# Optimization experiments

Hardware: AMD Instinct MI355X
Metric: run time of the kernel (lower is better)

The kernel has to match this reference:

```python
import jax, jax.numpy as jnp
import numpy as np

B, L, N, D = 256, 200, 256, 16
K = 8  # fixed dopri5 substeps per output interval (replaces adaptive step control)
LN_EPS = 1e-5


def setup_inputs() -> dict:
    key = jax.random.key(0)
    ks = jax.random.split(key, 16)

    def w(k, i, o):
        return (jax.random.normal(k, (i, o), jnp.float32) / np.float32(np.sqrt(i)))

    return {
        "x_seq": jax.random.normal(ks[0], (B, L, N), jnp.float32),
        "tvec": jnp.arange(L, dtype=jnp.float32) * 0.05,
        "eps": jax.random.normal(ks[1], (B, D), jnp.float32),
        # encoder
        "enc_w1": w(ks[2], N, 512), "enc_b1": jnp.zeros((512,), jnp.float32),
        "enc_w2": w(ks[3], 512, 256), "enc_b2": jnp.zeros((256,), jnp.float32),
        "enc_w3": w(ks[4], 256, 128), "enc_b3": jnp.zeros((128,), jnp.float32),
        "mu_w": w(ks[5], 128, D), "mu_b": jnp.zeros((D,), jnp.float32),
        "lv_w": w(ks[6], 128, D), "lv_b": jnp.zeros((D,), jnp.float32),
        # latent ODE func
        "ode_w1": w(ks[7], D, 128), "ode_b1": jnp.zeros((128,), jnp.float32),
        "ode_w2": w(ks[8], 128, 128), "ode_b2": jnp.zeros((128,), jnp.float32),
        "ode_w3": w(ks[9], 128, D), "ode_b3": jnp.zeros((D,), jnp.float32),
        "ln_g": jnp.ones((D,), jnp.float32), "ln_b": jnp.zeros((D,), jnp.float32),
        # decoder
        "dec_w1": w(ks[10], D, 512), "dec_b1": jnp.zeros((512,), jnp.float32),
        "dec_w2": w(ks[11], 512, 512), "dec_b2": jnp.zeros((512,), jnp.float32),
        "dec_w3": w(ks[12], 512, N), "dec_b3": jnp.zeros((N,), jnp.float32),
    }


def _forward(x_seq, tvec, eps,
             enc_w1, enc_b1, enc_w2, enc_b2, enc_w3, enc_b3,
             mu_w, mu_b, lv_w, lv_b,
             ode_w1, ode_b1, ode_w2, ode_b2, ode_w3, ode_b3, ln_g, ln_b,
             dec_w1, dec_b1, dec_w2, dec_b2, dec_w3, dec_b3):
    # ---- encode x0 -> (mu, logvar), reparameterize ----
    x0 = x_seq[:, 0, :]                                   # [B, N]
    h = jax.nn.relu(x0 @ enc_w1 + enc_b1)
    h = jax.nn.relu(h @ enc_w2 + enc_b2)
    h = jax.nn.relu(h @ enc_w3 + enc_b3)
    mu = h @ mu_w + mu_b                                  # [B, D]
    logvar = h @ lv_w + lv_b                              # [B, D]
    z0 = mu + jnp.exp(0.5 * logvar) * eps                 # [B, D]

    # ---- latent ODE dynamics f(z) (t-independent) ----
    def f(z):
        a = jax.nn.silu(z @ ode_w1 + ode_b1)
        a = jax.nn.silu(a @ ode_w2 + ode_b2)
        dz = a @ ode_w3 + ode_b3
        m = jnp.mean(dz, axis=-1, keepdims=True)
        v = jnp.mean(jnp.square(dz - m), axis=-1, keepdims=True)
        return (dz - m) * jax.lax.rsqrt(v + LN_EPS) * ln_g + ln_b

    # ---- dopri5 (RK45) step with step size hstep ----
    def dopri_step(z, hstep):
        k1 = f(z)
        k2 = f(z + hstep * (k1 / 5.0))
        k3 = f(z + hstep * (3.0 / 40.0 * k1 + 9.0 / 40.0 * k2))
        k4 = f(z + hstep * (44.0 / 45.0 * k1 - 56.0 / 15.0 * k2 + 32.0 / 9.0 * k3))
        k5 = f(z + hstep * (19372.0 / 6561.0 * k1 - 25360.0 / 2187.0 * k2
                            + 64448.0 / 6561.0 * k3 - 212.0 / 729.0 * k4))
        k6 = f(z + hstep * (9017.0 / 3168.0 * k1 - 355.0 / 33.0 * k2
                            + 46732.0 / 5247.0 * k3 + 49.0 / 176.0 * k4
                            - 5103.0 / 18656.0 * k5))
        return z + hstep * (35.0 / 384.0 * k1 + 500.0 / 1113.0 * k3
                            + 125.0 / 192.0 * k4 - 2187.0 / 6784.0 * k5
                            + 11.0 / 84.0 * k6)

    dts = tvec[1:] - tvec[:-1]                            # [L-1]

    def interval(z, dt):
        hsub = dt / K
        def sub(zc, _):
            return dopri_step(zc, hsub), None
        z_next, _ = jax.lax.scan(sub, z, None, length=K)
        return z_next, z_next

    _, zs = jax.lax.scan(interval, z0, dts)               # [L-1, B, D]
    z_traj = jnp.concatenate([z0[None], zs], axis=0)      # [L, B, D]
    z_traj = jnp.transpose(z_traj, (1, 0, 2))             # [B, L, D]

    dt3 = dts.reshape(1, -1, 1)
    zdiff = (z_traj[:, 1:, :] - z_traj[:, :-1, :]) / dt3  # [B, L-1, D]

    # ---- decode trajectory ----
    g = jax.nn.relu(z_traj @ dec_w1 + dec_b1)
    g = jax.nn.relu(g @ dec_w2 + dec_b2)
    xhat = g @ dec_w3 + dec_b3                            # [B, L, N]
    return xhat, mu, logvar, z_traj, zdiff


def reference(x_seq, tvec, eps,
              enc_w1, enc_b1, enc_w2, enc_b2, enc_w3, enc_b3,
              mu_w, mu_b, lv_w, lv_b,
              ode_w1, ode_b1, ode_w2, ode_b2, ode_w3, ode_b3, ln_g, ln_b,
              dec_w1, dec_b1, dec_w2, dec_b2, dec_w3, dec_b3):
    return _forward(x_seq, tvec, eps,
                    enc_w1, enc_b1, enc_w2, enc_b2, enc_w3, enc_b3,
                    mu_w, mu_b, lv_w, lv_b,
                    ode_w1, ode_b1, ode_w2, ode_b2, ode_w3, ode_b3, ln_g, ln_b,
                    dec_w1, dec_b1, dec_w2, dec_b2, dec_w3, dec_b3)
```

## Files before the change

kernel.cpp:

```cpp
#include <hip/hip_runtime.h>

#define OFF_MU   13107200
#define OFF_LV   13111296
#define OFF_ZT   13115392
#define OFF_ZD   13934592

typedef float v2f __attribute__((ext_vector_type(2)));

__device__ __forceinline__ float silu_f(float x) {
    return x / (1.0f + __expf(-x));
}

__device__ __forceinline__ float readlane_f(float v, int l) {
    return __uint_as_float(__builtin_amdgcn_readlane(__float_as_uint(v), l));
}

__device__ __forceinline__ v2f fma2(v2f a, v2f b, v2f c) {
    return __builtin_elementwise_fma(a, b, c);
}

template <int CTRL>
__device__ __forceinline__ float dppadd(float x) {
    int y = __builtin_amdgcn_update_dpp(0, __float_as_int(x), CTRL, 0xF, 0xF, true);
    return x + __int_as_float(y);
}

__device__ __forceinline__ float sum16_dpp(float x) {
    x = dppadd<0xB1>(x);
    x = dppadd<0x4E>(x);
    x = dppadd<0x141>(x);
    x = dppadd<0x140>(x);
    return x;
}

__global__ __launch_bounds__(256) void enc_kernel(
    const float* __restrict__ xseq, const float* __restrict__ eps,
    const float* __restrict__ w1, const float* __restrict__ b1,
    const float* __restrict__ w2, const float* __restrict__ b2,
    const float* __restrict__ w3, const float* __restrict__ b3,
    const float* __restrict__ muw, const float* __restrict__ mub,
    const float* __restrict__ lvw, const float* __restrict__ lvb,
    float* __restrict__ out)
{
    __shared__ float xr[256];
    __shared__ float h1[512];
    __shared__ float h2[256];
    __shared__ float h3[128];

    const int t = threadIdx.x;
    const int b = blockIdx.x;

    xr[t] = xseq[b * (200 * 256) + t];
    __syncthreads();

    {
        float acc0 = b1[t], acc1 = b1[t + 256];
        for (int i = 0; i < 256; ++i) {
            float xv = xr[i];
            acc0 = fmaf(xv, w1[i * 512 + t],       acc0);
            acc1 = fmaf(xv, w1[i * 512 + t + 256], acc1);
        }
        h1[t]       = fmaxf(acc0, 0.0f);
        h1[t + 256] = fmaxf(acc1, 0.0f);
    }
    __syncthreads();

    {
        float acc = b2[t];
        for (int i = 0; i < 512; ++i) acc = fmaf(h1[i], w2[i * 256 + t], acc);
        h2[t] = fmaxf(acc, 0.0f);
    }
    __syncthreads();

    if (t < 128) {
        float acc = b3[t];
        for (int i = 0; i < 256; ++i) acc = fmaf(h2[i], w3[i * 128 + t], acc);
        h3[t] = fmaxf(acc, 0.0f);
    }
    __syncthreads();

    if (t < 16) {
        float mu = mub[t], lv = lvb[t];
        for (int i = 0; i < 128; ++i) {
            float hv = h3[i];
            mu = fmaf(hv, muw[i * 16 + t], mu);
            lv = fmaf(hv, lvw[i * 16 + t], lv);
        }
        out[OFF_MU + b * 16 + t] = mu;
        out[OFF_LV + b * 16 + t] = lv;
        float z0 = mu + __expf(0.5f * lv) * eps[b * 16 + t];
        out[OFF_ZT + b * 3200 + t] = z0;
    }
}

__global__ __launch_bounds__(256, 1) void ode_kernel(
    const float* __restrict__ tvec,
    const float* __restrict__ ow1, const float* __restrict__ ob1,
    const float* __restrict__ ow2, const float* __restrict__ ob2,
    const float* __restrict__ ow3, const float* __restrict__ ob3,
    const float* __restrict__ lng, const float* __restrict__ lnb,
    float* __restrict__ out)
{
    __shared__ __align__(16) float a1s[4][32];
    __shared__ __align__(16) float part[4 * 128];
    __shared__ __align__(16) float a2s[128];
    __shared__ __align__(16) float p3s[4 * 64];

    const int tid  = threadIdx.x;
    const int wv   = tid >> 6;
    const int lane = tid & 63;
    const int b    = blockIdx.x;
    const int d    = lane & 15;
    const int g    = lane >> 4;
    const int c0   = lane, c1 = lane + 64;
    const int col1 = 32 * wv + (lane & 31);

    const volatile float* vw1 = ow1;
    const volatile float* vw2 = ow2;
    const volatile float* vw3 = ow3;

    float w1r[16];
#pragma unroll
    for (int k = 0; k < 16; ++k) w1r[k] = vw1[k * 128 + col1];

    v2f w2r0[16], w2r1[16];
#pragma unroll
    for (int q = 0; q < 16; ++q) {
        int k0 = 32 * wv + 2 * q;
        v2f t0 = { vw2[k0 * 128 + c0], vw2[(k0 + 1) * 128 + c0] };
        v2f t1 = { vw2[k0 * 128 + c1], vw2[(k0 + 1) * 128 + c1] };
        w2r0[q] = t0;
        w2r1[q] = t1;
    }
    v2f w3r[16];
#pragma unroll
    for (int qq = 0; qq < 8; ++qq) {
        int qsel = (qq + 2 * g) & 7;
        int k0   = 32 * g + 4 * qsel;
        v2f t0 = { vw3[(k0 + 0) * 16 + d], vw3[(k0 + 1) * 16 + d] };
        v2f t1 = { vw3[(k0 + 2) * 16 + d], vw3[(k0 + 3) * 16 + d] };
        w3r[2 * qq]     = t0;
        w3r[2 * qq + 1] = t1;
    }
    const volatile float* vb1 = ob1;
    const volatile float* vb2 = ob2;
    const volatile float* vb3 = ob3;
    const volatile float* vlg = lng;
    const volatile float* vlb = lnb;
    const float b1c  = vb1[col1];
    const float b2t  = vb2[tid & 127];
    const float b3d  = vb3[d];
    const float lngd = vlg[d], lnbd = vlb[d];

    float* ztraj = out + OFF_ZT + b * 3200;
    float* zdiff = out + OFF_ZD + b * 3184;

    float z = ztraj[d];

    auto feval = [&](float za) -> float {
        float ae = 0.0f, ao = 0.0f;
#pragma unroll
        for (int k = 0; k < 16; k += 2) {
            float zk0 = readlane_f(za, k);
            float zk1 = readlane_f(za, k + 1);
            ae = fmaf(zk0, w1r[k],     ae);
            ao = fmaf(zk1, w1r[k + 1], ao);
        }
        if (lane < 32) a1s[wv][lane] = silu_f(ae + ao + b1c);

        v2f A  = {0.0f, 0.0f}, Ab = {0.0f, 0.0f};
        v2f B  = {0.0f, 0.0f}, Bb = {0.0f, 0.0f};
        const float4* a14 = (const float4*)a1s[wv];
#pragma unroll
        for (int i = 0; i < 8; ++i) {
            float4 av = a14[i];
            v2f plo = { av.x, av.y };
            v2f phi = { av.z, av.w };
            A  = fma2(plo, w2r0[2 * i],     A);
            Ab = fma2(phi, w2r0[2 * i + 1], Ab);
            B  = fma2(plo, w2r1[2 * i],     B);
            Bb = fma2(phi, w2r1[2 * i + 1], Bb);
        }
        part[wv * 128 + c0] = A.x + A.y + Ab.x + Ab.y;
        part[wv * 128 + c1] = B.x + B.y + Bb.x + Bb.y;
        __syncthreads();

        if (tid < 128) {
            float s = part[tid] + part[128 + tid]
                    + part[256 + tid] + part[384 + tid] + b2t;
            a2s[tid] = silu_f(s);
        }
        __syncthreads();

        v2f pp = {0.0f, 0.0f};
#pragma unroll
        for (int qq = 0; qq < 8; ++qq) {
            int qsel = (qq + 2 * g) & 7;
            float4 av = *(const float4*)&a2s[32 * g + 4 * qsel];
            pp = fma2((v2f){ av.x, av.y }, w3r[2 * qq],     pp);
            pp = fma2((v2f){ av.z, av.w }, w3r[2 * qq + 1], pp);
        }
        p3s[wv * 64 + lane] = pp.x + pp.y;
        const int pb = wv * 64 + d;
        float dz = b3d + p3s[pb] + p3s[pb + 16] + p3s[pb + 32] + p3s[pb + 48];

        float s1 = sum16_dpp(dz);
        float s2 = sum16_dpp(dz * dz);
        float m  = s1 * 0.0625f;
        float v  = fmaf(m, -m, s2 * 0.0625f);
        return (dz - m) * rsqrtf(v + 1e-5f) * lngd + lnbd;
    };

    for (int l = 0; l < 199; ++l) {
        const float dt = tvec[l + 1] - tvec[l];
        const float h  = dt * 0.125f;
        const float zstart = z;
        for (int s = 0; s < 8; ++s) {
            float k1 = feval(z);
            float k2 = feval(z + h * (k1 * (float)(1.0 / 5.0)));
            float k3 = feval(z + h * ((float)(3.0 / 40.0) * k1 + (float)(9.0 / 40.0) * k2));
            float k4 = feval(z + h * ((float)(44.0 / 45.0) * k1 - (float)(56.0 / 15.0) * k2
                                    + (float)(32.0 / 9.0) * k3));
            float k5 = feval(z + h * ((float)(19372.0 / 6561.0) * k1 - (float)(25360.0 / 2187.0) * k2
                                    + (float)(64448.0 / 6561.0) * k3 - (float)(212.0 / 729.0) * k4));
            float k6 = feval(z + h * ((float)(9017.0 / 3168.0) * k1 - (float)(355.0 / 33.0) * k2
                                    + (float)(46732.0 / 5247.0) * k3 + (float)(49.0 / 176.0) * k4
                                    - (float)(5103.0 / 18656.0) * k5));
            z = z + h * ((float)(35.0 / 384.0) * k1 + (float)(500.0 / 1113.0) * k3
                       + (float)(125.0 / 192.0) * k4 - (float)(2187.0 / 6784.0) * k5
                       + (float)(11.0 / 84.0) * k6);
        }
        if (tid < 16) {
            ztraj[(l + 1) * 16 + tid] = z;
            zdiff[l * 16 + tid] = (z - zstart) / dt;
        }
    }
}

#define GS 516

__global__ __launch_bounds__(256, 4) void dec_kernel(
    const float* __restrict__ ztr,
    const float* __restrict__ w1, const float* __restrict__ b1,
    const float* __restrict__ w2, const float* __restrict__ b2,
    const float* __restrict__ w3, const float* __restrict__ b3,
    float* __restrict__ xhat)
{
    __shared__ __align__(16) float zt[16 * 17];
    __shared__ __align__(16) float g[16 * GS];

    const int t    = threadIdx.x;
    const int blk  = blockIdx.x;
    const int tr   = t >> 5;
    const int tc   = t & 31;
    const int row0 = blk * 16;
    const int r0   = 2 * tr;

    {
        int r = t >> 4, dd = t & 15;
        zt[r * 17 + dd] = ztr[(row0 + r) * 16 + dd];
    }
    __syncthreads();

    {
        float acc[2][16];
#pragma unroll
        for (int p = 0; p < 2; ++p)
#pragma unroll
            for (int i = 0; i < 16; ++i) acc[p][i] = 0.0f;

#pragma unroll
        for (int k = 0; k < 16; ++k) {
            float a0 = zt[(r0 + 0) * 17 + k];
            float a1 = zt[(r0 + 1) * 17 + k];
            const float4* wr = (const float4*)(w1 + k * 512 + 16 * tc);
#pragma unroll
            for (int u = 0; u < 4; ++u) {
                float4 wv = wr[u];
                acc[0][4 * u + 0] = fmaf(a0, wv.x, acc[0][4 * u + 0]);
                acc[0][4 * u + 1] = fmaf(a0, wv.y, acc[0][4 * u + 1]);
                acc[0][4 * u + 2] = fmaf(a0, wv.z, acc[0][4 * u + 2]);
                acc[0][4 * u + 3] = fmaf(a0, wv.w, acc[0][4 * u + 3]);
                acc[1][4 * u + 0] = fmaf(a1, wv.x, acc[1][4 * u + 0]);
                acc[1][4 * u + 1] = fmaf(a1, wv.y, acc[1][4 * u + 1]);
                acc[1][4 * u + 2] = fmaf(a1, wv.z, acc[1][4 * u + 2]);
                acc[1][4 * u + 3] = fmaf(a1, wv.w, acc[1][4 * u + 3]);
            }
        }
        const float4* bb = (const float4*)(b1 + 16 * tc);
#pragma unroll
        for (int u = 0; u < 4; ++u) {
            float4 bv = bb[u];
#pragma unroll
            for (int p = 0; p < 2; ++p) {
                g[(r0 + p) * GS + 16 * tc + 4 * u + 0] = fmaxf(acc[p][4 * u + 0] + bv.x, 0.0f);
                g[(r0 + p) * GS + 16 * tc + 4 * u + 1] = fmaxf(acc[p][4 * u + 1] + bv.y, 0.0f);
                g[(r0 + p) * GS + 16 * tc + 4 * u + 2] = fmaxf(acc[p][4 * u + 2] + bv.z, 0.0f);
                g[(r0 + p) * GS + 16 * tc + 4 * u + 3] = fmaxf(acc[p][4 * u + 3] + bv.w, 0.0f);
            }
        }
    }
    __syncthreads();

    {
        float accB[2][16];
#pragma unroll
        for (int p = 0; p < 2; ++p)
#pragma unroll
            for (int i = 0; i < 16; ++i) accB[p][i] = 0.0f;

        for (int k4 = 0; k4 < 128; ++k4) {
            float4 av0 = *(const float4*)&g[(r0 + 0) * GS + 4 * k4];
            float4 av1 = *(const float4*)&g[(r0 + 1) * GS + 4 * k4];
            float a0[4] = {av0.x, av0.y, av0.z, av0.w};
            float a1[4] = {av1.x, av1.y, av1.z, av1.w};
#pragma unroll
            for (int u = 0; u < 4; ++u) {
                const float4* wr = (const float4*)(w2 + (4 * k4 + u) * 512 + 16 * tc);
#pragma unroll
                for (int q = 0; q < 4; ++q) {
                    float4 wv = wr[q];
                    accB[0][4 * q + 0] = fmaf(a0[u], wv.x, accB[0][4 * q + 0]);
                    accB[0][4 * q + 1] = fmaf(a0[u], wv.y, accB[0][4 * q + 1]);
                    accB[0][4 * q + 2] = fmaf(a0[u], wv.z, accB[0][4 * q + 2]);
                    accB[0][4 * q + 3] = fmaf(a0[u], wv.w, accB[0][4 * q + 3]);
                    accB[1][4 * q + 0] = fmaf(a1[u], wv.x, accB[1][4 * q + 0]);
                    accB[1][4 * q + 1] = fmaf(a1[u], wv.y, accB[1][4 * q + 1]);
                    accB[1][4 * q + 2] = fmaf(a1[u], wv.z, accB[1][4 * q + 2]);
                    accB[1][4 * q + 3] = fmaf(a1[u], wv.w, accB[1][4 * q + 3]);
                }
            }
        }
        __syncthreads();
        const float4* bb = (const float4*)(b2 + 16 * tc);
#pragma unroll
        for (int u = 0; u < 4; ++u) {
            float4 bv = bb[u];
#pragma unroll
            for (int p = 0; p < 2; ++p) {
                g[(r0 + p) * GS + 16 * tc + 4 * u + 0] = fmaxf(accB[p][4 * u + 0] + bv.x, 0.0f);
                g[(r0 + p) * GS + 16 * tc + 4 * u + 1] = fmaxf(accB[p][4 * u + 1] + bv.y, 0.0f);
                g[(r0 + p) * GS + 16 * tc + 4 * u + 2] = fmaxf(accB[p][4 * u + 2] + bv.z, 0.0f);
                g[(r0 + p) * GS + 16 * tc + 4 * u + 3] = fmaxf(accB[p][4 * u + 3] + bv.w, 0.0f);
            }
        }
    }
    __syncthreads();

    {
        float accC[2][8];
#pragma unroll
        for (int p = 0; p < 2; ++p)
#pragma unroll
            for (int i = 0; i < 8; ++i) accC[p][i] = 0.0f;

        for (int k4 = 0; k4 < 128; ++k4) {
            float4 av0 = *(const float4*)&g[(r0 + 0) * GS + 4 * k4];
            float4 av1 = *(const float4*)&g[(r0 + 1) * GS + 4 * k4];
            float a0[4] = {av0.x, av0.y, av0.z, av0.w};
            float a1[4] = {av1.x, av1.y, av1.z, av1.w};
#pragma unroll
            for (int u = 0; u < 4; ++u) {
                const float4* wr = (const float4*)(w3 + (4 * k4 + u) * 256 + 8 * tc);
                float4 w0 = wr[0], w1v = wr[1];
                accC[0][0] = fmaf(a0[u], w0.x,  accC[0][0]);
                accC[0][1] = fmaf(a0[u], w0.y,  accC[0][1]);
                accC[0][2] = fmaf(a0[u], w0.z,  accC[0][2]);
                accC[0][3] = fmaf(a0[u], w0.w,  accC[0][3]);
                accC[0][4] = fmaf(a0[u], w1v.x, accC[0][4]);
                accC[0][5] = fmaf(a0[u], w1v.y, accC[0][5]);
                accC[0][6] = fmaf(a0[u], w1v.z, accC[0][6]);
                accC[0][7] = fmaf(a0[u], w1v.w, accC[0][7]);
                accC[1][0] = fmaf(a1[u], w0.x,  accC[1][0]);
                accC[1][1] = fmaf(a1[u], w0.y,  accC[1][1]);
                accC[1][2] = fmaf(a1[u], w0.z,  accC[1][2]);
                accC[1][3] = fmaf(a1[u], w0.w,  accC[1][3]);
                accC[1][4] = fmaf(a1[u], w1v.x, accC[1][4]);
                accC[1][5] = fmaf(a1[u], w1v.y, accC[1][5]);
                accC[1][6] = fmaf(a1[u], w1v.z, accC[1][6]);
                accC[1][7] = fmaf(a1[u], w1v.w, accC[1][7]);
            }
        }
        const float4* bb = (const float4*)(b3 + 8 * tc);
        float4 bv0 = bb[0], bv1 = bb[1];
#pragma unroll
        for (int p = 0; p < 2; ++p) {
            float4 o0 = make_float4(accC[p][0] + bv0.x, accC[p][1] + bv0.y,
                                    accC[p][2] + bv0.z, accC[p][3] + bv0.w);
            float4 o1 = make_float4(accC[p][4] + bv1.x, accC[p][5] + bv1.y,
                                    accC[p][6] + bv1.z, accC[p][7] + bv1.w);
            float* dst = xhat + (size_t)(row0 + r0 + p) * 256 + 8 * tc;
            *(float4*)(dst)     = o0;
            *(float4*)(dst + 4) = o1;
        }
    }
}

extern "C" void kernel_launch(void* const* d_in, const int* in_sizes, int n_in,
                              void* d_out, int out_size, void* d_ws, size_t ws_size,
                              hipStream_t stream) {
    const float* x_seq  = (const float*)d_in[0];
    const float* tvec   = (const float*)d_in[1];
    const float* eps    = (const float*)d_in[2];
    const float* enc_w1 = (const float*)d_in[3];
    const float* enc_b1 = (const float*)d_in[4];
    const float* enc_w2 = (const float*)d_in[5];
    const float* enc_b2 = (const float*)d_in[6];
    const float* enc_w3 = (const float*)d_in[7];
    const float* enc_b3 = (const float*)d_in[8];
    const float* mu_w   = (const float*)d_in[9];
    const float* mu_b   = (const float*)d_in[10];
    const float* lv_w   = (const float*)d_in[11];
    const float* lv_b   = (const float*)d_in[12];
    const float* ode_w1 = (const float*)d_in[13];
    const float* ode_b1 = (const float*)d_in[14];
    const float* ode_w2 = (const float*)d_in[15];
    const float* ode_b2 = (const float*)d_in[16];
    const float* ode_w3 = (const float*)d_in[17];
    const float* ode_b3 = (const float*)d_in[18];
    const float* ln_g   = (const float*)d_in[19];
    const float* ln_b   = (const float*)d_in[20];
    const float* dec_w1 = (const float*)d_in[21];
    const float* dec_b1 = (const float*)d_in[22];
    const float* dec_w2 = (const float*)d_in[23];
    const float* dec_b2 = (const float*)d_in[24];
    const float* dec_w3 = (const float*)d_in[25];
    const float* dec_b3 = (const float*)d_in[26];
    float* out = (float*)d_out;

    enc_kernel<<<256, 256, 0, stream>>>(x_seq, eps, enc_w1, enc_b1, enc_w2, enc_b2,
                                        enc_w3, enc_b3, mu_w, mu_b, lv_w, lv_b, out);
    ode_kernel<<<256, 256, 0, stream>>>(tvec, ode_w1, ode_b1, ode_w2, ode_b2,
                                        ode_w3, ode_b3, ln_g, ln_b, out);
    dec_kernel<<<3200, 256, 0, stream>>>(out + OFF_ZT, dec_w1, dec_b1, dec_w2, dec_b2,
                                         dec_w3, dec_b3, out);
}
```

Before: 8.946 ms.

## Process two batch rows per ODE block to interleave independent RK chains

Each ODE workgroup now integrates two batch elements at once, sharing the register-resident weights and the barriers, and launches half as many blocks. Two independent dependency chains are interleaved inside each function evaluation to hide latency in the serial, barrier-bound RK loop. The cost is that only 128 workgroups run on a 256-CU part, so half the device sits idle, and register pressure rises.

Result: slower. 12.67 ms (+41.6%).

```diff
diff --git a/kernel.cpp b/kernel.cpp
--- a/kernel.cpp
+++ b/kernel.cpp
@@ -101,10 +101,10 @@
     const float* __restrict__ lng, const float* __restrict__ lnb,
     float* __restrict__ out)
 {
-    __shared__ __align__(16) float a1s[4][32];
-    __shared__ __align__(16) float part[4 * 128];
-    __shared__ __align__(16) float a2s[128];
-    __shared__ __align__(16) float p3s[4 * 64];
+    __shared__ __align__(16) float a1s[2][4][32];
+    __shared__ __align__(16) float part[2][4 * 128];
+    __shared__ __align__(16) float a2s[2][128];
+    __shared__ __align__(16) float p3s[2][4 * 64];
 
     const int tid  = threadIdx.x;
     const int wv   = tid >> 6;
@@ -152,87 +152,138 @@
     const float b3d  = vb3[d];
     const float lngd = vlg[d], lnbd = vlb[d];
 
-    float* ztraj = out + OFF_ZT + b * 3200;
-    float* zdiff = out + OFF_ZD + b * 3184;
-
-    float z = ztraj[d];
-
-    auto feval = [&](float za) -> float {
-        float ae = 0.0f, ao = 0.0f;
+    float* ztrajA = out + OFF_ZT + (2 * b)     * 3200;
+    float* ztrajB = out + OFF_ZT + (2 * b + 1) * 3200;
+    float* zdiffA = out + OFF_ZD + (2 * b)     * 3184;
+    float* zdiffB = out + OFF_ZD + (2 * b + 1) * 3184;
+
+    float zA = ztrajA[d];
+    float zB = ztrajB[d];
+
+    auto feval2 = [&](float zaA, float zaB, float& rA, float& rB) {
+        float aeA = 0.0f, aoA = 0.0f, aeB = 0.0f, aoB = 0.0f;
 #pragma unroll
         for (int k = 0; k < 16; k += 2) {
-            float zk0 = readlane_f(za, k);
-            float zk1 = readlane_f(za, k + 1);
-            ae = fmaf(zk0, w1r[k],     ae);
-            ao = fmaf(zk1, w1r[k + 1], ao);
-        }
-        if (lane < 32) a1s[wv][lane] = silu_f(ae + ao + b1c);
-
-        v2f A  = {0.0f, 0.0f}, Ab = {0.0f, 0.0f};
-        v2f B  = {0.0f, 0.0f}, Bb = {0.0f, 0.0f};
-        const float4* a14 = (const float4*)a1s[wv];
+            float zA0 = readlane_f(zaA, k);
+            float zA1 = readlane_f(zaA, k + 1);
+            float zB0 = readlane_f(zaB, k);
+            float zB1 = readlane_f(zaB, k + 1);
+            aeA = fmaf(zA0, w1r[k],     aeA);
+            aoA = fmaf(zA1, w1r[k + 1], aoA);
+            aeB = fmaf(zB0, w1r[k],     aeB);
+            aoB = fmaf(zB1, w1r[k + 1], aoB);
+        }
+        if (lane < 32) {
+            a1s[0][wv][lane & 31] = silu_f(aeA + aoA + b1c);
+            a1s[1][wv][lane & 31] = silu_f(aeB + aoB + b1c);
+        }
+
+        v2f AA = {0.f,0.f}, AAb = {0.f,0.f}, BA = {0.f,0.f}, BAb = {0.f,0.f};
+        v2f AB = {0.f,0.f}, ABb = {0.f,0.f}, BB = {0.f,0.f}, BBb = {0.f,0.f};
+        const float4* a4A = (const float4*)a1s[0][wv];
+        const float4* a4B = (const float4*)a1s[1][wv];
 #pragma unroll
         for (int i = 0; i < 8; ++i) {
-            float4 av = a14[i];
-            v2f plo = { av.x, av.y };
-            v2f phi = { av.z, av.w };
-            A  = fma2(plo, w2r0[2 * i],     A);
-            Ab = fma2(phi, w2r0[2 * i + 1], Ab);
-            B  = fma2(plo, w2r1[2 * i],     B);
-            Bb = fma2(phi, w2r1[2 * i + 1], Bb);
-        }
-        part[wv * 128 + c0] = A.x + A.y + Ab.x + Ab.y;
-        part[wv * 128 + c1] = B.x + B.y + Bb.x + Bb.y;
+            float4 avA = a4A[i];
+            float4 avB = a4B[i];
+            v2f pAl = { avA.x, avA.y }, pAh = { avA.z, avA.w };
+            v2f pBl = { avB.x, avB.y }, pBh = { avB.z, avB.w };
+            AA  = fma2(pAl, w2r0[2 * i],     AA);
+            AAb = fma2(pAh, w2r0[2 * i + 1], AAb);
+            BA  = fma2(pAl, w2r1[2 * i],     BA);
+            BAb = fma2(pAh, w2r1[2 * i + 1], BAb);
+            AB  = fma2(pBl, w2r0[2 * i],     AB);
+            ABb = fma2(pBh, w2r0[2 * i + 1], ABb);
+            BB  = fma2(pBl, w2r1[2 * i],     BB);
+            BBb = fma2(pBh, w2r1[2 * i + 1], BBb);
+        }
+        part[0][wv * 128 + c0] = AA.x + AA.y + AAb.x + AAb.y;
+        part[0][wv * 128 + c1] = BA.x + BA.y + BAb.x + BAb.y;
+        part[1][wv * 128 + c0] = AB.x + AB.y + ABb.x + ABb.y;
+        part[1][wv * 128 + c1] = BB.x + BB.y + BBb.x + BBb.y;
         __syncthreads();
 
-        if (tid < 128) {
-            float s = part[tid] + part[128 + tid]
-                    + part[256 + tid] + part[384 + tid] + b2t;
-            a2s[tid] = silu_f(s);
+        {
+            const int e  = tid >> 7;
+            const int t2 = tid & 127;
+            float s = part[e][t2] + part[e][128 + t2]
+                    + part[e][256 + t2] + part[e][384 + t2] + b2t;
+            a2s[e][t2] = silu_f(s);
         }
         __syncthreads();
 
-        v2f pp = {0.0f, 0.0f};
+        v2f ppA = {0.f, 0.f}, ppB = {0.f, 0.f};
 #pragma unroll
         for (int qq = 0; qq < 8; ++qq) {
             int qsel = (qq + 2 * g) & 7;
-            float4 av = *(const float4*)&a2s[32 * g + 4 * qsel];
-            pp = fma2((v2f){ av.x, av.y }, w3r[2 * qq],     pp);
-            pp = fma2((v2f){ av.z, av.w }, w3r[2 * qq + 1], pp);
-        }
-        p3s[wv * 64 + lane] = pp.x + pp.y;
+            float4 avA = *(const float4*)&a2s[0][32 * g + 4 * qsel];
+            float4 avB = *(const float4*)&a2s[1][32 * g + 4 * qsel];
+            ppA = fma2((v2f){ avA.x, avA.y }, w3r[2 * qq],     ppA);
+            ppA = fma2((v2f){ avA.z, avA.w }, w3r[2 * qq + 1], ppA);
+            ppB = fma2((v2f){ avB.x, avB.y }, w3r[2 * qq],     ppB);
+            ppB = fma2((v2f){ avB.z, avB.w }, w3r[2 * qq + 1], ppB);
+        }
+        p3s[0][wv * 64 + lane] = ppA.x + ppA.y;
+        p3s[1][wv * 64 + lane] = ppB.x + ppB.y;
         const int pb = wv * 64 + d;
-        float dz = b3d + p3s[pb] + p3s[pb + 16] + p3s[pb + 32] + p3s[pb + 48];
-
-        float s1 = sum16_dpp(dz);
-        float s2 = sum16_dpp(dz * dz);
-        float m  = s1 * 0.0625f;
-        float v  = fmaf(m, -m, s2 * 0.0625f);
-        return (dz - m) * rsqrtf(v + 1e-5f) * lngd + lnbd;
+        float dzA = b3d + p3s[0][pb] + p3s[0][pb + 16]
+                        + p3s[0][pb + 32] + p3s[0][pb + 48];
+        float dzB = b3d + p3s[1][pb] + p3s[1][pb + 16]
+                        + p3s[1][pb + 32] + p3s[1][pb + 48];
+
+        float s1A = sum16_dpp(dzA);
+        float s2A = sum16_dpp(dzA * dzA);
+        float s1B = sum16_dpp(dzB);
+        float s2B = sum16_dpp(dzB * dzB);
+        float mA  = s1A * 0.0625f;
+        float mB  = s1B * 0.0625f;
+        float vA  = fmaf(mA, -mA, s2A * 0.0625f);
+        float vB  = fmaf(mB, -mB, s2B * 0.0625f);
+        rA = (dzA - mA) * rsqrtf(vA + 1e-5f) * lngd + lnbd;
+        rB = (dzB - mB) * rsqrtf(vB + 1e-5f) * lngd + lnbd;
     };
 
     for (int l = 0; l < 199; ++l) {
         const float dt = tvec[l + 1] - tvec[l];
         const float h  = dt * 0.125f;
-        const float zstart = z;
+        const float zsA = zA, zsB = zB;
         for (int s = 0; s < 8; ++s) {
-            float k1 = feval(z);
-            float k2 = feval(z + h * (k1 * (float)(1.0 / 5.0)));
-            float k3 = feval(z + h * ((float)(3.0 / 40.0) * k1 + (float)(9.0 / 40.0) * k2));
-            float k4 = feval(z + h * ((float)(44.0 / 45.0) * k1 - (float)(56.0 / 15.0) * k2
-                                    + (float)(32.0 / 9.0) * k3));
-            float k5 = feval(z + h * ((float)(19372.0 / 6561.0) * k1 - (float)(25360.0 / 2187.0) * k2
-                                    + (float)(64448.0 / 6561.0) * k3 - (float)(212.0 / 729.0) * k4));
-            float k6 = feval(z + h * ((float)(9017.0 / 3168.0) * k1 - (float)(355.0 / 33.0) * k2
-                                    + (float)(46732.0 / 5247.0) * k3 + (float)(49.0 / 176.0) * k4
-                                    - (float)(5103.0 / 18656.0) * k5));
-            z = z + h * ((float)(35.0 / 384.0) * k1 + (float)(500.0 / 1113.0) * k3
-                       + (float)(125.0 / 192.0) * k4 - (float)(2187.0 / 6784.0) * k5
-                       + (float)(11.0 / 84.0) * k6);
+            float k1A, k1B, k2A, k2B, k3A, k3B, k4A, k4B, k5A, k5B, k6A, k6B;
+            feval2(zA, zB, k1A, k1B);
+            feval2(zA + h * (k1A * (float)(1.0 / 5.0)),
+                   zB + h * (k1B * (float)(1.0 / 5.0)), k2A, k2B);
+            feval2(zA + h * ((float)(3.0 / 40.0) * k1A + (float)(9.0 / 40.0) * k2A),
+                   zB + h * ((float)(3.0 / 40.0) * k1B + (float)(9.0 / 40.0) * k2B), k3A, k3B);
+            feval2(zA + h * ((float)(44.0 / 45.0) * k1A - (float)(56.0 / 15.0) * k2A
+                           + (float)(32.0 / 9.0) * k3A),
+                   zB + h * ((float)(44.0 / 45.0) * k1B - (float)(56.0 / 15.0) * k2B
+                           + (float)(32.0 / 9.0) * k3B), k4A, k4B);
+            feval2(zA + h * ((float)(19372.0 / 6561.0) * k1A - (float)(25360.0 / 2187.0) * k2A
+                           + (float)(64448.0 / 6561.0) * k3A - (float)(212.0 / 729.0) * k4A),
+                   zB + h * ((float)(19372.0 / 6561.0) * k1B - (float)(25360.0 / 2187.0) * k2B
+                           + (float)(64448.0 / 6561.0) * k3B - (float)(212.0 / 729.0) * k4B),
+                   k5A, k5B);
+            feval2(zA + h * ((float)(9017.0 / 3168.0) * k1A - (float)(355.0 / 33.0) * k2A
+                           + (float)(46732.0 / 5247.0) * k3A + (float)(49.0 / 176.0) * k4A
+                           - (float)(5103.0 / 18656.0) * k5A),
+                   zB + h * ((float)(9017.0 / 3168.0) * k1B - (float)(355.0 / 33.0) * k2B
+                           + (float)(46732.0 / 5247.0) * k3B + (float)(49.0 / 176.0) * k4B
+                           - (float)(5103.0 / 18656.0) * k5B),
+                   k6A, k6B);
+            zA = zA + h * ((float)(35.0 / 384.0) * k1A + (float)(500.0 / 1113.0) * k3A
+                         + (float)(125.0 / 192.0) * k4A - (float)(2187.0 / 6784.0) * k5A
+                         + (float)(11.0 / 84.0) * k6A);
+            zB = zB + h * ((float)(35.0 / 384.0) * k1B + (float)(500.0 / 1113.0) * k3B
+                         + (float)(125.0 / 192.0) * k4B - (float)(2187.0 / 6784.0) * k5B
+                         + (float)(11.0 / 84.0) * k6B);
         }
         if (tid < 16) {
-            ztraj[(l + 1) * 16 + tid] = z;
-            zdiff[l * 16 + tid] = (z - zstart) / dt;
+            ztrajA[(l + 1) * 16 + tid] = zA;
+            zdiffA[l * 16 + tid] = (zA - zsA) / dt;
+        } else if (tid >= 128 && tid < 144) {
+            const int t2 = tid - 128;
+            ztrajB[(l + 1) * 16 + t2] = zB;
+            zdiffB[l * 16 + t2] = (zB - zsB) / dt;
         }
     }
 }
@@ -430,7 +481,7 @@
 
     enc_kernel<<<256, 256, 0, stream>>>(x_seq, eps, enc_w1, enc_b1, enc_w2, enc_b2,
                                         enc_w3, enc_b3, mu_w, mu_b, lv_w, lv_b, out);
-    ode_kernel<<<256, 256, 0, stream>>>(tvec, ode_w1, ode_b1, ode_w2, ode_b2,
+    ode_kernel<<<128, 256, 0, stream>>>(tvec, ode_w1, ode_b1, ode_w2, ode_b2,
                                         ode_w3, ode_b3, ln_g, ln_b, out);
     dec_kernel<<<3200, 256, 0, stream>>>(out + OFF_ZT, dec_w1, dec_b1, dec_w2, dec_b2,
                                          dec_w3, dec_b3, out);
```

## Pack two batch rows per ODE block and drop one barrier per eval

Applied to the files above, without the earlier changes.

The ODE kernel now runs two batch elements per 512-thread block, 128 blocks in total, with each group of four waves handling one element. The second __syncthreads per function evaluation is removed: every wave redundantly reduces the layer-2 partial sums into its own private a2 buffer. The partial-sum buffer is double-buffered by evaluation parity so the single remaining barrier is enough. This halves the block count, which may leave CUs idle on a 256-CU part, and adds redundant reduction work per wave in exchange for fewer barriers.

After: 10.72 ms. +19.9%, slower.

```diff
diff --git a/kernel.cpp b/kernel.cpp
--- a/kernel.cpp
+++ b/kernel.cpp
@@ -93,7 +93,7 @@
     }
 }
 
-__global__ __launch_bounds__(256, 1) void ode_kernel(
+__global__ __launch_bounds__(512, 1) void ode_kernel(
     const float* __restrict__ tvec,
     const float* __restrict__ ow1, const float* __restrict__ ob1,
     const float* __restrict__ ow2, const float* __restrict__ ob2,
@@ -101,19 +101,21 @@
     const float* __restrict__ lng, const float* __restrict__ lnb,
     float* __restrict__ out)
 {
-    __shared__ __align__(16) float a1s[4][32];
-    __shared__ __align__(16) float part[4 * 128];
-    __shared__ __align__(16) float a2s[128];
-    __shared__ __align__(16) float p3s[4 * 64];
+    __shared__ __align__(16) float a1s[2][4][32];
+    __shared__ __align__(16) float part[2][2][512];
+    __shared__ __align__(16) float a2w[2][4][128];
+    __shared__ __align__(16) float p3s[2][4][64];
 
     const int tid  = threadIdx.x;
     const int wv   = tid >> 6;
+    const int e    = wv >> 2;
+    const int kq   = wv & 3;
     const int lane = tid & 63;
     const int b    = blockIdx.x;
     const int d    = lane & 15;
     const int g    = lane >> 4;
     const int c0   = lane, c1 = lane + 64;
-    const int col1 = 32 * wv + (lane & 31);
+    const int col1 = 32 * kq + (lane & 31);
 
     const volatile float* vw1 = ow1;
     const volatile float* vw2 = ow2;
@@ -126,7 +128,7 @@
     v2f w2r0[16], w2r1[16];
 #pragma unroll
     for (int q = 0; q < 16; ++q) {
-        int k0 = 32 * wv + 2 * q;
+        int k0 = 32 * kq + 2 * q;
         v2f t0 = { vw2[k0 * 128 + c0], vw2[(k0 + 1) * 128 + c0] };
         v2f t1 = { vw2[k0 * 128 + c1], vw2[(k0 + 1) * 128 + c1] };
         w2r0[q] = t0;
@@ -148,16 +150,16 @@
     const volatile float* vlg = lng;
     const volatile float* vlb = lnb;
     const float b1c  = vb1[col1];
-    const float b2t  = vb2[tid & 127];
+    const float b2c0 = vb2[c0], b2c1 = vb2[c1];
     const float b3d  = vb3[d];
     const float lngd = vlg[d], lnbd = vlb[d];
 
-    float* ztraj = out + OFF_ZT + b * 3200;
-    float* zdiff = out + OFF_ZD + b * 3184;
+    float* ztraj = out + OFF_ZT + (2 * b + e) * 3200;
+    float* zdiff = out + OFF_ZD + (2 * b + e) * 3184;
 
     float z = ztraj[d];
 
-    auto feval = [&](float za) -> float {
+    auto feval = [&](float za, int p) -> float {
         float ae = 0.0f, ao = 0.0f;
 #pragma unroll
         for (int k = 0; k < 16; k += 2) {
@@ -166,11 +168,11 @@
             ae = fmaf(zk0, w1r[k],     ae);
             ao = fmaf(zk1, w1r[k + 1], ao);
         }
-        if (lane < 32) a1s[wv][lane] = silu_f(ae + ao + b1c);
+        if (lane < 32) a1s[e][kq][lane] = silu_f(ae + ao + b1c);
 
         v2f A  = {0.0f, 0.0f}, Ab = {0.0f, 0.0f};
         v2f B  = {0.0f, 0.0f}, Bb = {0.0f, 0.0f};
-        const float4* a14 = (const float4*)a1s[wv];
+        const float4* a14 = (const float4*)a1s[e][kq];
 #pragma unroll
         for (int i = 0; i < 8; ++i) {
             float4 av = a14[i];
@@ -181,28 +183,30 @@
             B  = fma2(plo, w2r1[2 * i],     B);
             Bb = fma2(phi, w2r1[2 * i + 1], Bb);
         }
-        part[wv * 128 + c0] = A.x + A.y + Ab.x + Ab.y;
-        part[wv * 128 + c1] = B.x + B.y + Bb.x + Bb.y;
+        part[p][e][kq * 128 + c0] = A.x + A.y + Ab.x + Ab.y;
+        part[p][e][kq * 128 + c1] = B.x + B.y + Bb.x + Bb.y;
         __syncthreads();
 
-        if (tid < 128) {
-            float s = part[tid] + part[128 + tid]
-                    + part[256 + tid] + part[384 + tid] + b2t;
-            a2s[tid] = silu_f(s);
-        }
-        __syncthreads();
+        {
+            float s0 = part[p][e][c0] + part[p][e][128 + c0]
+                     + part[p][e][256 + c0] + part[p][e][384 + c0] + b2c0;
+            float s1 = part[p][e][c1] + part[p][e][128 + c1]
+                     + part[p][e][256 + c1] + part[p][e][384 + c1] + b2c1;
+            a2w[e][kq][c0 & 127] = silu_f(s0);
+            a2w[e][kq][c1 & 127] = silu_f(s1);
+        }
 
         v2f pp = {0.0f, 0.0f};
 #pragma unroll
         for (int qq = 0; qq < 8; ++qq) {
             int qsel = (qq + 2 * g) & 7;
-            float4 av = *(const float4*)&a2s[32 * g + 4 * qsel];
+            float4 av = *(const float4*)&a2w[e][kq][32 * g + 4 * qsel];
             pp = fma2((v2f){ av.x, av.y }, w3r[2 * qq],     pp);
             pp = fma2((v2f){ av.z, av.w }, w3r[2 * qq + 1], pp);
         }
-        p3s[wv * 64 + lane] = pp.x + pp.y;
-        const int pb = wv * 64 + d;
-        float dz = b3d + p3s[pb] + p3s[pb + 16] + p3s[pb + 32] + p3s[pb + 48];
+        p3s[e][kq][lane] = pp.x + pp.y;
+        float dz = b3d + p3s[e][kq][d] + p3s[e][kq][d + 16]
+                       + p3s[e][kq][d + 32] + p3s[e][kq][d + 48];
 
         float s1 = sum16_dpp(dz);
         float s2 = sum16_dpp(dz * dz);
@@ -216,23 +220,23 @@
         const float h  = dt * 0.125f;
         const float zstart = z;
         for (int s = 0; s < 8; ++s) {
-            float k1 = feval(z);
-            float k2 = feval(z + h * (k1 * (float)(1.0 / 5.0)));
-            float k3 = feval(z + h * ((float)(3.0 / 40.0) * k1 + (float)(9.0 / 40.0) * k2));
+            float k1 = feval(z, 0);
+            float k2 = feval(z + h * (k1 * (float)(1.0 / 5.0)), 1);
+            float k3 = feval(z + h * ((float)(3.0 / 40.0) * k1 + (float)(9.0 / 40.0) * k2), 0);
             float k4 = feval(z + h * ((float)(44.0 / 45.0) * k1 - (float)(56.0 / 15.0) * k2
-                                    + (float)(32.0 / 9.0) * k3));
+                                    + (float)(32.0 / 9.0) * k3), 1);
             float k5 = feval(z + h * ((float)(19372.0 / 6561.0) * k1 - (float)(25360.0 / 2187.0) * k2
-                                    + (float)(64448.0 / 6561.0) * k3 - (float)(212.0 / 729.0) * k4));
+                                    + (float)(64448.0 / 6561.0) * k3 - (float)(212.0 / 729.0) * k4), 0);
             float k6 = feval(z + h * ((float)(9017.0 / 3168.0) * k1 - (float)(355.0 / 33.0) * k2
                                     + (float)(46732.0 / 5247.0) * k3 + (float)(49.0 / 176.0) * k4
-                                    - (float)(5103.0 / 18656.0) * k5));
+                                    - (float)(5103.0 / 18656.0) * k5), 1);
             z = z + h * ((float)(35.0 / 384.0) * k1 + (float)(500.0 / 1113.0) * k3
                        + (float)(125.0 / 192.0) * k4 - (float)(2187.0 / 6784.0) * k5
                        + (float)(11.0 / 84.0) * k6);
         }
-        if (tid < 16) {
-            ztraj[(l + 1) * 16 + tid] = z;
-            zdiff[l * 16 + tid] = (z - zstart) / dt;
+        if (kq == 0 && lane < 16) {
+            ztraj[(l + 1) * 16 + lane] = z;
+            zdiff[l * 16 + lane] = (z - zstart) / dt;
         }
     }
 }
@@ -430,7 +434,7 @@
 
     enc_kernel<<<256, 256, 0, stream>>>(x_seq, eps, enc_w1, enc_b1, enc_w2, enc_b2,
                                         enc_w3, enc_b3, mu_w, mu_b, lv_w, lv_b, out);
-    ode_kernel<<<256, 256, 0, stream>>>(tvec, ode_w1, ode_b1, ode_w2, ode_b2,
+    ode_kernel<<<128, 512, 0, stream>>>(tvec, ode_w1, ode_b1, ode_w2, ode_b2,
                                         ode_w3, ode_b3, ln_g, ln_b, out);
     dec_kernel<<<3200, 256, 0, stream>>>(out + OFF_ZT, dec_w1, dec_b1, dec_w2, dec_b2,
                                          dec_w3, dec_b3, out);
```
